# Performance work log

Hardware: AMD Instinct MI355X
Metric: run time of the kernel (lower is better)

Reference implementation:

```python
import jax, jax.numpy as jnp
import numpy as np

B, T, SC, D, N, K, H = 2, 1024, 1024, 2048, 16, 4, 128
SOFTCAP = 50.0
BIG_NEG = -2.3819763e38


def _apply_rope(x, positions, max_wavelength=10_000):
    # x: [B, T, heads, H], positions: [B, T]
    h = x.shape[-1]
    freq_exponents = (2.0 / h) * jnp.arange(h // 2, dtype=jnp.float32)
    timescale = max_wavelength ** freq_exponents
    radians = positions[..., None].astype(jnp.float32) / timescale  # [B,T,H/2]
    radians = radians[..., None, :]  # [B,T,1,H/2]
    sin, cos = jnp.sin(radians), jnp.cos(radians)
    x1, x2 = jnp.split(x, 2, axis=-1)
    out = jnp.concatenate([x1 * cos - x2 * sin, x2 * cos + x1 * sin], axis=-1)
    return out.astype(x.dtype)


def setup_inputs() -> dict:
    key = jax.random.key(0)
    ks = jax.random.split(key, 6)
    x = jax.random.normal(ks[0], (B, T, D), jnp.float32)
    # new-token positions follow the cache: SC .. SC+T-1
    positions = jnp.broadcast_to(SC + jnp.arange(T, dtype=jnp.int32), (B, T))
    # causal mask over concatenated [cache | new] keys
    q_pos = SC + jnp.arange(T)
    k_pos = jnp.arange(SC + T)
    attn_mask = jnp.broadcast_to(
        (k_pos[None, :] <= q_pos[:, None])[None, None], (B, 1, T, SC + T)
    )
    cache_k = jax.random.normal(ks[1], (B, SC, K, H), jnp.float32)
    cache_v = jax.random.normal(ks[2], (B, SC, K, H), jnp.float32)
    wq = jax.random.normal(ks[3], (N, D, H), jnp.float32) * (D ** -0.5)
    wkv = jax.random.normal(ks[4], (2, K, D, H), jnp.float32) * (D ** -0.5)
    wout = jax.random.normal(ks[5], (N, H, D), jnp.float32) * ((N * H) ** -0.5)
    return {"x": x, "positions": positions, "attn_mask": attn_mask,
            "cache_k": cache_k, "cache_v": cache_v,
            "wq": wq, "wkv": wkv, "wout": wout}


def reference(x, positions, attn_mask, cache_k, cache_v, wq, wkv, wout):
    dtype = x.dtype
    h = wq.shape[-1]
    k_heads = wkv.shape[1]
    # projections (GQA path: separate q and fused kv einsums)
    q = jnp.einsum('BTD,NDH->BTNH', x, wq.astype(dtype))
    kv = jnp.einsum('BSD,cKDH->cBSKH', x, wkv.astype(dtype))
    k, v = kv[0], kv[1]
    # RoPE then query pre-attn scaling (rsqrt_head_dim)
    q = _apply_rope(q, positions) * (h ** -0.5)
    k = _apply_rope(k, positions)
    # KV cache concat along sequence axis
    k = jnp.concatenate([cache_k.astype(dtype), k], axis=1)
    v = jnp.concatenate([cache_v.astype(dtype), v], axis=1)
    b, t, n, _ = q.shape
    g = n // k_heads
    q = q.reshape(b, t, k_heads, g, h)  # B T K G H
    logits = jnp.einsum('BTKGH,BSKH->BKGTS', q, k,
                        preferred_element_type=jnp.float32)
    # tanh logits softcap
    logits = jnp.tanh(logits / SOFTCAP) * SOFTCAP
    masked = jnp.where(attn_mask[:, :, None, :, :], logits, BIG_NEG)
    probs = jax.nn.softmax(masked, axis=-1).astype(dtype)
    encoded = jnp.einsum('BKGTS,BSKH->BTKGH', probs, v)
    encoded = encoded.reshape(b, t, n, h)
    out = jnp.einsum('BTNH,NHD->BTD', encoded, wout.astype(dtype))
    return out
```

## Files before the change

kernel.cpp:

```cpp
#include <hip/hip_runtime.h>
#include <stdint.h>
#include <stddef.h>


typedef __bf16 bf16_t;
typedef __bf16 bf16x8 __attribute__((ext_vector_type(8)));
typedef __bf16 bf16x4 __attribute__((ext_vector_type(4)));
typedef float  f32x4  __attribute__((ext_vector_type(4)));

#define GLDS16(gsrc, ldst)                                                      \
  __builtin_amdgcn_global_load_lds(                                             \
      (const __attribute__((address_space(1))) void*)(gsrc),                    \
      (__attribute__((address_space(3))) void*)(ldst), 16, 0, 0)

__global__ void k_cast_bf16(const float* __restrict__ src, bf16_t* __restrict__ dst, int n4) {
  int i = blockIdx.x * 256 + threadIdx.x;
  if (i >= n4) return;
  f32x4 v = *(const f32x4*)(src + (size_t)i * 4);
  bf16x4 o;
  o[0] = (bf16_t)v[0]; o[1] = (bf16_t)v[1]; o[2] = (bf16_t)v[2]; o[3] = (bf16_t)v[3];
  *(bf16x4*)(dst + (size_t)i * 4) = o;
}

__global__ void k_transpose_cast(const float* __restrict__ src, bf16_t* __restrict__ dst,
                                 int R, int C, size_t sz, size_t dz) {
  __shared__ bf16_t tile[64][65];
  const float* s = src + (size_t)blockIdx.z * sz;
  bf16_t* d = dst + (size_t)blockIdx.z * dz;
  const int c0 = blockIdx.x * 64, r0 = blockIdx.y * 64;
  const int tid = threadIdx.x;
#pragma unroll
  for (int it = 0; it < 16; ++it) {
    int idx = it * 256 + tid;
    int rl = idx >> 6, cl = idx & 63;
    tile[rl][cl] = (bf16_t)s[(size_t)(r0 + rl) * C + (c0 + cl)];
  }
  __syncthreads();
#pragma unroll
  for (int it = 0; it < 16; ++it) {
    int idx = it * 256 + tid;
    int cl = idx >> 6, rl = idx & 63;
    d[(size_t)(c0 + cl) * R + (r0 + rl)] = tile[rl][cl];
  }
}

__global__ __launch_bounds__(512)
void k_gemm_bt(const bf16_t* __restrict__ A, const bf16_t* __restrict__ Bt,
               float* __restrict__ C, int M, int N, int Kd) {
  __shared__ char gsm[65536];
  const int tid = threadIdx.x;
  const int w = tid >> 6, l = tid & 63;
  const int wq = w & 3, wr = wq >> 1, wc = wq & 1, wk = w >> 2;
  const int lr = l & 15, lk = l >> 4;
  const int nwg = gridDim.x * gridDim.y;
  const int bid = blockIdx.y * gridDim.x + blockIdx.x;
  const int cpx = nwg >> 3;
  const int sid = (bid & 7) * cpx + (bid >> 3);
  const int row0 = (sid % gridDim.x) * 128;
  const int col0 = (sid / gridDim.x) * 128;

  auto stage = [&](int buf, int k0) {
#pragma unroll
    for (int inst = 0; inst < 2; ++inst) {
      uint32_t oo = (uint32_t)(inst * 8192 + tid * 16);
      uint32_t r  = oo >> 7;
      uint32_t kb = (oo ^ (((oo >> 7) & 7u) << 4)) & 127u;
      GLDS16((const char*)(A + (size_t)(row0 + r) * Kd + k0) + kb,
             gsm + buf * 16384 + oo);
      GLDS16((const char*)(Bt + (size_t)(col0 + r) * Kd + k0) + kb,
             gsm + 32768 + buf * 16384 + oo);
    }
  };

  f32x4 acc[4][4] = {};
  stage(0, 0);
  asm volatile("s_waitcnt vmcnt(0)" ::: "memory");
  __builtin_amdgcn_s_barrier();
  int cur = 0;
  for (int k0 = 0; k0 < Kd; k0 += 64) {
    const int kn = (k0 + 64 < Kd) ? (k0 + 64) : k0;
    stage(cur ^ 1, kn);
    const char* Ab = gsm + cur * 16384;
    const char* Bb = gsm + 32768 + cur * 16384;
    bf16x8 af[4], bfr[4];
#pragma unroll
    for (int m = 0; m < 4; ++m) {
      uint32_t r = (uint32_t)(wr * 64 + m * 16 + lr);
      uint32_t a = (r * 128u + (uint32_t)(wk * 64 + lk * 16)) ^ ((r & 7u) << 4);
      af[m] = *(const bf16x8*)(Ab + a);
    }
#pragma unroll
    for (int n = 0; n < 4; ++n) {
      uint32_t r = (uint32_t)(wc * 64 + n * 16 + lr);
      uint32_t a = (r * 128u + (uint32_t)(wk * 64 + lk * 16)) ^ ((r & 7u) << 4);
      bfr[n] = *(const bf16x8*)(Bb + a);
    }
    __builtin_amdgcn_s_setprio(1);
#pragma unroll
    for (int m = 0; m < 4; ++m)
#pragma unroll
      for (int n = 0; n < 4; ++n)
        acc[m][n] = __builtin_amdgcn_mfma_f32_16x16x32_bf16(af[m], bfr[n], acc[m][n], 0, 0, 0);
    __builtin_amdgcn_s_setprio(0);
    asm volatile("s_waitcnt vmcnt(0)" ::: "memory");
    __builtin_amdgcn_s_barrier();
    __builtin_amdgcn_sched_barrier(0);
    cur ^= 1;
  }
  if (wk == 1) {
#pragma unroll
    for (int m = 0; m < 4; ++m)
#pragma unroll
      for (int n = 0; n < 4; ++n)
        *(f32x4*)(gsm + wq * 16384 + ((m * 4 + n) * 64 + l) * 16) = acc[m][n];
  }
  __syncthreads();
  if (wk == 0) {
#pragma unroll
    for (int m = 0; m < 4; ++m) {
      const int rr = row0 + wr * 64 + m * 16 + lk * 4;
#pragma unroll
      for (int n = 0; n < 4; ++n) {
        f32x4 o = *(const f32x4*)(gsm + wq * 16384 + ((m * 4 + n) * 64 + l) * 16);
        const int cc = col0 + wc * 64 + n * 16 + lr;
        float* cp = C + (size_t)rr * N + cc;
#pragma unroll
        for (int j = 0; j < 4; ++j) cp[(size_t)j * N] = acc[m][n][j] + o[j];
      }
    }
  }
}

__global__ void k_rope(const float* __restrict__ qkv, const int* __restrict__ positions,
                       bf16_t* __restrict__ Qr, bf16_t* __restrict__ Kf) {
  const int row = blockIdx.x;
  const int b = row >> 10, t = row & 1023;
  const int tid = threadIdx.x;
  __shared__ float cs[64], sn[64];
  if (tid < 64) {
    float fe = (float)tid * (2.0f / 128.0f);
    float ts = powf(10000.0f, fe);
    float rad = (float)positions[row] / ts;
    sn[tid] = sinf(rad);
    cs[tid] = cosf(rad);
  }
  __syncthreads();
  const float* rowp = qkv + (size_t)row * 3072;
  const float qs = 0.08838834764831845f;
#pragma unroll
  for (int it = 0; it < 8; ++it) {
    int idx = it * 256 + tid;
    int n = idx >> 7, hh = idx & 127;
    int hp = hh & 63;
    float x1 = rowp[n * 128 + hp];
    float x2 = rowp[n * 128 + 64 + hp];
    float o = (hh < 64) ? (x1 * cs[hp] - x2 * sn[hp]) : (x2 * cs[hp] + x1 * sn[hp]);
    Qr[(((size_t)b * 16 + n) * 1024 + t) * 128 + hh] = (bf16_t)(o * qs);
  }
#pragma unroll
  for (int it = 0; it < 2; ++it) {
    int idx = it * 256 + tid;
    int kh = idx >> 7, hh = idx & 127;
    int hp = hh & 63;
    float x1 = rowp[2048 + kh * 128 + hp];
    float x2 = rowp[2048 + kh * 128 + 64 + hp];
    float o = (hh < 64) ? (x1 * cs[hp] - x2 * sn[hp]) : (x2 * cs[hp] + x1 * sn[hp]);
    Kf[(((size_t)b * 4 + kh) * 2048 + 1024 + t) * 128 + hh] = (bf16_t)o;
  }
}

__global__ void k_cache_k(const float* __restrict__ ck, bf16_t* __restrict__ Kf) {
  const int row = blockIdx.x;
  const int b = row >> 10, s = row & 1023;
  const float* src = ck + (size_t)row * 512;
  const int tid = threadIdx.x;
#pragma unroll
  for (int it = 0; it < 2; ++it) {
    int idx = it * 256 + tid;
    int kh = idx >> 7, hh = idx & 127;
    Kf[(((size_t)b * 4 + kh) * 2048 + s) * 128 + hh] = (bf16_t)src[idx];
  }
}

__global__ void k_build_vt(const float* __restrict__ cv, const float* __restrict__ qkv,
                           bf16_t* __restrict__ Vt) {
  __shared__ bf16_t vt[64][129];
  const int s0 = blockIdx.x * 64;
  const int bk = blockIdx.y;
  const int b = bk >> 2, kh = bk & 3;
  const int tid = threadIdx.x;
#pragma unroll
  for (int it = 0; it < 32; ++it) {
    int idx = it * 256 + tid;
    int sl = idx >> 7, hh = idx & 127;
    int s = s0 + sl;
    float v = (s < 1024)
      ? cv[(((size_t)b * 1024 + s) * 4 + kh) * 128 + hh]
      : qkv[((size_t)b * 1024 + (s - 1024)) * 3072 + 2560 + kh * 128 + hh];
    vt[sl][hh] = (bf16_t)v;
  }
  __syncthreads();
#pragma unroll
  for (int it = 0; it < 32; ++it) {
    int idx = it * 256 + tid;
    int hh = idx >> 6, sl = idx & 63;
    Vt[((size_t)bk * 128 + hh) * 2048 + s0 + sl] = vt[sl][hh];
  }
}

__global__ __launch_bounds__(512)
void k_attn(const bf16_t* __restrict__ Qr, const bf16_t* __restrict__ Kf,
            const bf16_t* __restrict__ Vt, bf16_t* __restrict__ enc) {
  __shared__ char smem[73728];
  const int bid = blockIdx.y * gridDim.x + blockIdx.x;
  const int sid = (bid & 7) * 64 + (bid >> 3);
  const int qsel = sid & 15;
  const int bn = sid >> 4;
  const int qblk = ((bn >> 1) & 1) ? (15 - qsel) : qsel;
  const int b = bn >> 4, n = bn & 15;
  const int kh = n >> 2;
  const int tid = threadIdx.x;
  const int w = tid >> 6, l = tid & 63;
  const int wqg = w & 3, ws = w >> 2;
  const int lr = l & 15, lk = l >> 4;
  const bf16_t* Kbase = Kf + ((size_t)b * 4 + kh) * 2048 * 128;
  const bf16_t* Vbase = Vt + ((size_t)b * 4 + kh) * 128 * 2048;

  const int tq = qblk * 64 + wqg * 16 + lr;
  const bf16_t* qp = Qr + ((size_t)bn * 1024 + tq) * 128;
  bf16x8 aq[4];
#pragma unroll
  for (int kk = 0; kk < 4; ++kk) aq[kk] = *(const bf16x8*)(qp + kk * 32 + lk * 8);

  auto stageK = [&](int buf, int s0) {
#pragma unroll
    for (int inst = 0; inst < 2; ++inst) {
      uint32_t oo = (uint32_t)(inst * 8192 + tid * 16);
      uint32_t r  = oo >> 8;
      uint32_t kb = (oo ^ (((oo >> 8) & 7u) << 4)) & 255u;
      GLDS16((const char*)(Kbase + (size_t)(s0 + r) * 128) + kb,
             smem + buf * 16384 + oo);
    }
  };
  auto stageV = [&](int buf, int s0) {
#pragma unroll
    for (int inst = 0; inst < 2; ++inst) {
      uint32_t oo = (uint32_t)(inst * 8192 + tid * 16);
      uint32_t r  = oo >> 7;
      uint32_t sb = (oo ^ (((oo >> 7) & 7u) << 4)) & 127u;
      GLDS16((const char*)(Vbase + (size_t)r * 2048 + s0) + sb,
             smem + 32768 + buf * 16384 + oo);
    }
  };

  char* pw = smem + 65536 + wqg * 2048;
  f32x4 acc[8] = {};
  float psum = 0.f;
  const int ntiles = 17 + qblk;
  const int qg2 = 1024 + tq;

  stageK(0, 0);
  stageV(0, 0);
  asm volatile("s_waitcnt vmcnt(0)" ::: "memory");
  __builtin_amdgcn_s_barrier();
  int cur = 0;

  for (int st = 0; st < ntiles; ++st) {
    const int s0 = st * 64;
    const int sn = (st + 1 < ntiles) ? (s0 + 64) : s0;
    stageK(cur ^ 1, sn);
    stageV(cur ^ 1, sn);
    const char* Kc = smem + cur * 16384;
    const char* Vc = smem + 32768 + cur * 16384;

    f32x4 sacc[2] = {};
    __builtin_amdgcn_s_setprio(1);
#pragma unroll
    for (int kk = 0; kk < 4; ++kk) {
#pragma unroll
      for (int sh = 0; sh < 2; ++sh) {
        uint32_t r = (uint32_t)((ws * 2 + sh) * 16 + lr);
        uint32_t a = (r * 256u + (uint32_t)(kk * 64 + lk * 16)) ^ ((r & 7u) << 4);
        bf16x8 ak = *(const bf16x8*)(Kc + a);
        sacc[sh] = __builtin_amdgcn_mfma_f32_16x16x32_bf16(ak, aq[kk], sacc[sh], 0, 0, 0);
      }
    }
    __builtin_amdgcn_s_setprio(0);

    const bool last = (st == ntiles - 1);
#pragma unroll
    for (int sh = 0; sh < 2; ++sh) {
      const int sf = ws * 2 + sh;
      bf16x4 pq;
#pragma unroll
      for (int j = 0; j < 4; ++j) {
        float lg = sacc[sh][j];
        float t  = lg * 1.4426950408889634f;
        float u  = 1.0f - (lg * lg) * (1.0f / 7500.0f);
        float p  = __builtin_amdgcn_exp2f(t * u);
        if (last) {
          int sg = s0 + sf * 16 + lk * 4 + j;
          if (sg > qg2) p = 0.0f;
        }
        psum += p;
        pq[j] = (bf16_t)p;
      }
      uint32_t a = ((uint32_t)(lr * 128) + (uint32_t)((sf * 16 + lk * 4) * 2)) ^ (((uint32_t)lr & 7u) << 4);
      *(bf16x4*)(pw + a) = pq;
    }
    asm volatile("s_waitcnt lgkmcnt(0)" ::: "memory");
    __builtin_amdgcn_sched_barrier(0);

    {
      uint32_t a = ((uint32_t)(lr * 128) + (uint32_t)(ws * 64 + lk * 16)) ^ (((uint32_t)lr & 7u) << 4);
      bf16x8 ap = *(const bf16x8*)(pw + a);
      __builtin_amdgcn_s_setprio(1);
#pragma unroll
      for (int hf = 0; hf < 8; ++hf) {
        uint32_t h = (uint32_t)(hf * 16 + lr);
        uint32_t va = (h * 128u + (uint32_t)(ws * 64 + lk * 16)) ^ ((h & 7u) << 4);
        bf16x8 bv = *(const bf16x8*)(Vc + va);
        acc[hf] = __builtin_amdgcn_mfma_f32_16x16x32_bf16(ap, bv, acc[hf], 0, 0, 0);
      }
      __builtin_amdgcn_s_setprio(0);
    }
    asm volatile("s_waitcnt vmcnt(0)" ::: "memory");
    __builtin_amdgcn_s_barrier();
    __builtin_amdgcn_sched_barrier(0);
    cur ^= 1;
  }

  float ps = psum;
  ps += __shfl_xor(ps, 16);
  ps += __shfl_xor(ps, 32);
  float* accL = (float*)smem;
  float* psL  = (float*)(smem + 65536);
  psL[wqg * 128 + ws * 64 + l] = ps;
  if (ws == 1) {
#pragma unroll
    for (int hf = 0; hf < 8; ++hf)
      *(f32x4*)(accL + wqg * 2048 + hf * 256 + l * 4) = acc[hf];
  }
  __syncthreads();
  if (ws == 0) {
    float tot = ps + psL[wqg * 128 + 64 + l];
    float inv = 1.0f / (tot + 1e-30f);
    float invj[4];
#pragma unroll
    for (int j = 0; j < 4; ++j) invj[j] = __shfl(inv, lk * 4 + j);
#pragma unroll
    for (int hf = 0; hf < 8; ++hf) {
      f32x4 o2 = *(const f32x4*)(accL + wqg * 2048 + hf * 256 + l * 4);
#pragma unroll
      for (int j = 0; j < 4; ++j) {
        int trow = qblk * 64 + wqg * 16 + lk * 4 + j;
        enc[((size_t)b * 1024 + trow) * 2048 + (n * 128 + hf * 16 + lr)] =
            (bf16_t)((acc[hf][j] + o2[j]) * invj[j]);
      }
    }
  }
}

extern "C" void kernel_launch(void* const* d_in, const int* in_sizes, int n_in,
                              void* d_out, int out_size, void* d_ws, size_t ws_size,
                              hipStream_t stream) {
  (void)in_sizes; (void)n_in; (void)out_size; (void)ws_size;
  const float* x    = (const float*)d_in[0];
  const int*   pos  = (const int*)d_in[1];
  const float* ck   = (const float*)d_in[3];
  const float* cv   = (const float*)d_in[4];
  const float* wq   = (const float*)d_in[5];
  const float* wkv  = (const float*)d_in[6];
  const float* wout = (const float*)d_in[7];
  float* out = (float*)d_out;

  char* p = (char*)d_ws;
  bf16_t* xb  = (bf16_t*)p; p += (size_t)2048 * 2048 * 2;
  bf16_t* w1t = (bf16_t*)p; p += (size_t)3072 * 2048 * 2;
  float*  qkv = (float*) p; p += (size_t)2048 * 3072 * 4;
  bf16_t* Qr  = (bf16_t*)p; p += (size_t)32 * 1024 * 128 * 2;
  bf16_t* Kf  = (bf16_t*)p; p += (size_t)8 * 2048 * 128 * 2;
  bf16_t* Vt  = (bf16_t*)p; p += (size_t)8 * 128 * 2048 * 2;
  bf16_t* enc = (bf16_t*)p; p += (size_t)2048 * 2048 * 2;
  bf16_t* wot = (bf16_t*)p; p += (size_t)2048 * 2048 * 2;

  k_cast_bf16<<<4096, 256, 0, stream>>>(x, xb, 1048576);
  k_transpose_cast<<<dim3(2, 32, 16), 256, 0, stream>>>(wq,  w1t, 2048, 128,
                                                        (size_t)2048 * 128, (size_t)128 * 2048);
  k_transpose_cast<<<dim3(2, 32, 8),  256, 0, stream>>>(wkv, w1t + (size_t)2048 * 2048, 2048, 128,
                                                        (size_t)2048 * 128, (size_t)128 * 2048);
  k_transpose_cast<<<dim3(32, 32, 1), 256, 0, stream>>>(wout, wot, 2048, 2048, 0, 0);
  k_gemm_bt<<<dim3(16, 24), 512, 0, stream>>>(xb, w1t, qkv, 2048, 3072, 2048);
  k_rope<<<2048, 256, 0, stream>>>(qkv, pos, Qr, Kf);
  k_cache_k<<<2048, 256, 0, stream>>>(ck, Kf);
  k_build_vt<<<dim3(32, 8), 256, 0, stream>>>(cv, qkv, Vt);
  k_attn<<<dim3(16, 32), 512, 0, stream>>>(Qr, Kf, Vt, enc);
  k_gemm_bt<<<dim3(16, 16), 512, 0, stream>>>(enc, wot, out, 2048, 2048, 2048);
}
```

Baseline: 143.9 us.

## Restructure attention warps to 32x32 MFMA for PV with four-way key split

The attention kernel's warp layout changes from 4 query groups by 2 key halves to 2 query groups of 32 rows by 4 key-slices of 16. Each K fragment load now feeds two QK MFMAs, and the PV product uses 32x32x16 MFMAs, which should reduce LDS reads per MFMA. The cross-warp reduction becomes a two-stage tree through shared memory with atomic row sums, adding extra barriers. It also adds an occupancy hint to launch_bounds and switches RoPE to fast exp2/sin/cos intrinsics, at some accuracy risk.

```diff
diff --git a/kernel.cpp b/kernel.cpp
--- a/kernel.cpp
+++ b/kernel.cpp
@@ -7,6 +7,7 @@
 typedef __bf16 bf16x8 __attribute__((ext_vector_type(8)));
 typedef __bf16 bf16x4 __attribute__((ext_vector_type(4)));
 typedef float  f32x4  __attribute__((ext_vector_type(4)));
+typedef float  f32x16 __attribute__((ext_vector_type(16)));
 
 #define GLDS16(gsrc, ldst)                                                      \
   __builtin_amdgcn_global_load_lds(                                             \
@@ -139,10 +140,9 @@
   __shared__ float cs[64], sn[64];
   if (tid < 64) {
     float fe = (float)tid * (2.0f / 128.0f);
-    float ts = powf(10000.0f, fe);
-    float rad = (float)positions[row] / ts;
-    sn[tid] = sinf(rad);
-    cs[tid] = cosf(rad);
+    float rad = (float)positions[row] * __builtin_amdgcn_exp2f(-fe * 13.287712379549449f);
+    sn[tid] = __sinf(rad);
+    cs[tid] = __cosf(rad);
   }
   __syncthreads();
   const float* rowp = qkv + (size_t)row * 3072;
@@ -208,7 +208,7 @@
   }
 }
 
-__global__ __launch_bounds__(512)
+__global__ __launch_bounds__(512, 4)
 void k_attn(const bf16_t* __restrict__ Qr, const bf16_t* __restrict__ Kf,
             const bf16_t* __restrict__ Vt, bf16_t* __restrict__ enc) {
   __shared__ char smem[73728];
@@ -221,16 +221,19 @@
   const int kh = n >> 2;
   const int tid = threadIdx.x;
   const int w = tid >> 6, l = tid & 63;
-  const int wqg = w & 3, ws = w >> 2;
+  const int qg = w & 1, sq = w >> 1;
   const int lr = l & 15, lk = l >> 4;
+  const int l31 = l & 31, l5 = l >> 5;
   const bf16_t* Kbase = Kf + ((size_t)b * 4 + kh) * 2048 * 128;
   const bf16_t* Vbase = Vt + ((size_t)b * 4 + kh) * 128 * 2048;
 
-  const int tq = qblk * 64 + wqg * 16 + lr;
-  const bf16_t* qp = Qr + ((size_t)bn * 1024 + tq) * 128;
-  bf16x8 aq[4];
-#pragma unroll
-  for (int kk = 0; kk < 4; ++kk) aq[kk] = *(const bf16x8*)(qp + kk * 32 + lk * 8);
+  bf16x8 aq[2][4];
+#pragma unroll
+  for (int qf = 0; qf < 2; ++qf) {
+    const bf16_t* qp = Qr + ((size_t)bn * 1024 + qblk * 64 + qg * 32 + qf * 16 + lr) * 128;
+#pragma unroll
+    for (int kk = 0; kk < 4; ++kk) aq[qf][kk] = *(const bf16x8*)(qp + kk * 32 + lk * 8);
+  }
 
   auto stageK = [&](int buf, int s0) {
 #pragma unroll
@@ -253,11 +256,11 @@
     }
   };
 
-  char* pw = smem + 65536 + wqg * 2048;
-  f32x4 acc[8] = {};
-  float psum = 0.f;
+  char* pw = smem + 65536 + w * 1024;
+  f32x16 acc[4] = {};
+  float psum[2] = {0.f, 0.f};
   const int ntiles = 17 + qblk;
-  const int qg2 = 1024 + tq;
+  const int qglob0 = 1024 + qblk * 64 + qg * 32 + lr;
 
   stageK(0, 0);
   stageV(0, 0);
@@ -277,50 +280,48 @@
     __builtin_amdgcn_s_setprio(1);
 #pragma unroll
     for (int kk = 0; kk < 4; ++kk) {
-#pragma unroll
-      for (int sh = 0; sh < 2; ++sh) {
-        uint32_t r = (uint32_t)((ws * 2 + sh) * 16 + lr);
-        uint32_t a = (r * 256u + (uint32_t)(kk * 64 + lk * 16)) ^ ((r & 7u) << 4);
-        bf16x8 ak = *(const bf16x8*)(Kc + a);
-        sacc[sh] = __builtin_amdgcn_mfma_f32_16x16x32_bf16(ak, aq[kk], sacc[sh], 0, 0, 0);
-      }
+      uint32_t r = (uint32_t)(sq * 16 + lr);
+      uint32_t a = (r * 256u + (uint32_t)(kk * 64 + lk * 16)) ^ ((r & 7u) << 4);
+      bf16x8 ak = *(const bf16x8*)(Kc + a);
+      sacc[0] = __builtin_amdgcn_mfma_f32_16x16x32_bf16(ak, aq[0][kk], sacc[0], 0, 0, 0);
+      sacc[1] = __builtin_amdgcn_mfma_f32_16x16x32_bf16(ak, aq[1][kk], sacc[1], 0, 0, 0);
     }
     __builtin_amdgcn_s_setprio(0);
 
     const bool last = (st == ntiles - 1);
 #pragma unroll
-    for (int sh = 0; sh < 2; ++sh) {
-      const int sf = ws * 2 + sh;
+    for (int qf = 0; qf < 2; ++qf) {
+      const int q = qf * 16 + lr;
       bf16x4 pq;
 #pragma unroll
       for (int j = 0; j < 4; ++j) {
-        float lg = sacc[sh][j];
+        float lg = sacc[qf][j];
         float t  = lg * 1.4426950408889634f;
         float u  = 1.0f - (lg * lg) * (1.0f / 7500.0f);
         float p  = __builtin_amdgcn_exp2f(t * u);
         if (last) {
-          int sg = s0 + sf * 16 + lk * 4 + j;
-          if (sg > qg2) p = 0.0f;
+          int sg = s0 + sq * 16 + lk * 4 + j;
+          if (sg > qglob0 + qf * 16) p = 0.0f;
         }
-        psum += p;
+        psum[qf] += p;
         pq[j] = (bf16_t)p;
       }
-      uint32_t a = ((uint32_t)(lr * 128) + (uint32_t)((sf * 16 + lk * 4) * 2)) ^ (((uint32_t)lr & 7u) << 4);
+      uint32_t a = (uint32_t)(q * 32) + (((uint32_t)(lk * 8)) ^ ((((uint32_t)q >> 2) & 1u) << 4));
       *(bf16x4*)(pw + a) = pq;
     }
     asm volatile("s_waitcnt lgkmcnt(0)" ::: "memory");
     __builtin_amdgcn_sched_barrier(0);
 
     {
-      uint32_t a = ((uint32_t)(lr * 128) + (uint32_t)(ws * 64 + lk * 16)) ^ (((uint32_t)lr & 7u) << 4);
-      bf16x8 ap = *(const bf16x8*)(pw + a);
+      uint32_t pa_a = (uint32_t)(l31 * 32) + (((uint32_t)(l5 * 16)) ^ ((((uint32_t)l31 >> 2) & 1u) << 4));
+      bf16x8 pa = *(const bf16x8*)(pw + pa_a);
       __builtin_amdgcn_s_setprio(1);
 #pragma unroll
-      for (int hf = 0; hf < 8; ++hf) {
-        uint32_t h = (uint32_t)(hf * 16 + lr);
-        uint32_t va = (h * 128u + (uint32_t)(ws * 64 + lk * 16)) ^ ((h & 7u) << 4);
-        bf16x8 bv = *(const bf16x8*)(Vc + va);
-        acc[hf] = __builtin_amdgcn_mfma_f32_16x16x32_bf16(ap, bv, acc[hf], 0, 0, 0);
+      for (int hf = 0; hf < 4; ++hf) {
+        uint32_t h = (uint32_t)(hf * 32 + l31);
+        uint32_t va = (h * 128u + (((uint32_t)(sq * 32 + l5 * 16)) ^ ((h & 7u) << 4)));
+        bf16x8 vb = *(const bf16x8*)(Vc + va);
+        acc[hf] = __builtin_amdgcn_mfma_f32_32x32x16_bf16(pa, vb, acc[hf], 0, 0, 0);
       }
       __builtin_amdgcn_s_setprio(0);
     }
@@ -330,32 +331,73 @@
     cur ^= 1;
   }
 
-  float ps = psum;
-  ps += __shfl_xor(ps, 16);
-  ps += __shfl_xor(ps, 32);
+  float ps0 = psum[0];
+  ps0 += __shfl_xor(ps0, 16); ps0 += __shfl_xor(ps0, 32);
+  float ps1 = psum[1];
+  ps1 += __shfl_xor(ps1, 16); ps1 += __shfl_xor(ps1, 32);
+  float* psL = (float*)(smem + 65536);
   float* accL = (float*)smem;
-  float* psL  = (float*)(smem + 65536);
-  psL[wqg * 128 + ws * 64 + l] = ps;
-  if (ws == 1) {
-#pragma unroll
-    for (int hf = 0; hf < 8; ++hf)
-      *(f32x4*)(accL + wqg * 2048 + hf * 256 + l * 4) = acc[hf];
-  }
-  __syncthreads();
-  if (ws == 0) {
-    float tot = ps + psL[wqg * 128 + 64 + l];
-    float inv = 1.0f / (tot + 1e-30f);
-    float invj[4];
-#pragma unroll
-    for (int j = 0; j < 4; ++j) invj[j] = __shfl(inv, lk * 4 + j);
-#pragma unroll
-    for (int hf = 0; hf < 8; ++hf) {
-      f32x4 o2 = *(const f32x4*)(accL + wqg * 2048 + hf * 256 + l * 4);
-#pragma unroll
-      for (int j = 0; j < 4; ++j) {
-        int trow = qblk * 64 + wqg * 16 + lk * 4 + j;
-        enc[((size_t)b * 1024 + trow) * 2048 + (n * 128 + hf * 16 + lr)] =
-            (bf16_t)((acc[hf][j] + o2[j]) * invj[j]);
+
+  if (tid < 64) psL[tid] = 0.f;
+  if (sq >= 2) {
+    const int slot = qg * 2 + (sq - 2);
+#pragma unroll
+    for (int hf = 0; hf < 4; ++hf)
+#pragma unroll
+      for (int c = 0; c < 4; ++c) {
+        f32x4 v; v[0] = acc[hf][c*4]; v[1] = acc[hf][c*4+1]; v[2] = acc[hf][c*4+2]; v[3] = acc[hf][c*4+3];
+        *(f32x4*)(accL + slot * 4096 + hf * 1024 + l * 16 + c * 4) = v;
+      }
+  }
+  __syncthreads();
+  if (l < 16) {
+    atomicAdd(&psL[qg * 32 + lr], ps0);
+    atomicAdd(&psL[qg * 32 + 16 + lr], ps1);
+  }
+  if (sq < 2) {
+    const int slot = qg * 2 + sq;
+#pragma unroll
+    for (int hf = 0; hf < 4; ++hf)
+#pragma unroll
+      for (int c = 0; c < 4; ++c) {
+        f32x4 v = *(const f32x4*)(accL + slot * 4096 + hf * 1024 + l * 16 + c * 4);
+        acc[hf][c*4] += v[0]; acc[hf][c*4+1] += v[1]; acc[hf][c*4+2] += v[2]; acc[hf][c*4+3] += v[3];
+      }
+  }
+  __syncthreads();
+  if (sq == 1) {
+    const int slot = qg * 2 + 1;
+#pragma unroll
+    for (int hf = 0; hf < 4; ++hf)
+#pragma unroll
+      for (int c = 0; c < 4; ++c) {
+        f32x4 v; v[0] = acc[hf][c*4]; v[1] = acc[hf][c*4+1]; v[2] = acc[hf][c*4+2]; v[3] = acc[hf][c*4+3];
+        *(f32x4*)(accL + slot * 4096 + hf * 1024 + l * 16 + c * 4) = v;
+      }
+  }
+  __syncthreads();
+  if (sq == 0) {
+    const int slot = qg * 2 + 1;
+#pragma unroll
+    for (int hf = 0; hf < 4; ++hf)
+#pragma unroll
+      for (int c = 0; c < 4; ++c) {
+        f32x4 v = *(const f32x4*)(accL + slot * 4096 + hf * 1024 + l * 16 + c * 4);
+        acc[hf][c*4] += v[0]; acc[hf][c*4+1] += v[1]; acc[hf][c*4+2] += v[2]; acc[hf][c*4+3] += v[3];
+      }
+    float invv[16];
+#pragma unroll
+    for (int r = 0; r < 16; ++r) {
+      int qrow = qg * 32 + (r & 3) + 8 * (r >> 2) + 4 * l5;
+      invv[r] = 1.0f / (psL[qrow] + 1e-30f);
+    }
+#pragma unroll
+    for (int hf = 0; hf < 4; ++hf) {
+#pragma unroll
+      for (int r = 0; r < 16; ++r) {
+        int trow = qblk * 64 + qg * 32 + (r & 3) + 8 * (r >> 2) + 4 * l5;
+        enc[((size_t)b * 1024 + trow) * 2048 + (n * 128 + hf * 32 + l31)] =
+            (bf16_t)(acc[hf][r] * invv[r]);
       }
     }
   }
```

Result: slower. 154.7 us (+7.5%).
